# Optimization experiments

Hardware: AMD Instinct MI355X
Metric: run time of the kernel (lower is better)

## Reference

```python
import jax, jax.numpy as jnp
import numpy as np

B = 32768      # batch
D_RGB = 512    # resnet18 feature dim (fc.in_features)
D_SPD = 128    # speed branch width
D_IN = D_RGB + D_SPD  # 640
H = 256        # branch MLP hidden/out width
C = 7          # number of command branches


def setup_inputs() -> dict:
    key = jax.random.key(0)
    ks = jax.random.split(key, 24)
    s = 0.05
    n = jax.random.normal
    inp = {
        "rgb_feat": n(ks[0], (B, D_RGB), jnp.float32),
        "spd": n(ks[1], (B, 1), jnp.float32),
        "cmd": jax.random.randint(ks[2], (B,), 0, C, jnp.int32),
        # speed input MLP: 1 -> 128 -> 128 -> 128, tanh
        "spd_W1": n(ks[3], (1, D_SPD), jnp.float32) * s,
        "spd_b1": jnp.zeros((D_SPD,), jnp.float32),
        "spd_W2": n(ks[4], (D_SPD, D_SPD), jnp.float32) * s,
        "spd_b2": jnp.zeros((D_SPD,), jnp.float32),
        "spd_W3": n(ks[5], (D_SPD, D_SPD), jnp.float32) * s,
        "spd_b3": jnp.zeros((D_SPD,), jnp.float32),
        # 7 branch MLPs (stacked): 640 -> 256 -> 256 -> 256, sigmoid after each
        "W1": n(ks[6], (C, D_IN, H), jnp.float32) * s,
        "b1": jnp.zeros((C, H), jnp.float32),
        "W2": n(ks[7], (C, H, H), jnp.float32) * s,
        "b2": jnp.zeros((C, H), jnp.float32),
        "W3": n(ks[8], (C, H, H), jnp.float32) * s,
        "b3": jnp.zeros((C, H), jnp.float32),
        # per-branch heads: Linear(256,1) + sigmoid/tanh/sigmoid
        "hW_brk": n(ks[9], (C, H, 1), jnp.float32) * s,
        "hb_brk": jnp.zeros((C, 1), jnp.float32),
        "hW_str": n(ks[10], (C, H, 1), jnp.float32) * s,
        "hb_str": jnp.zeros((C, 1), jnp.float32),
        "hW_thr": n(ks[11], (C, H, 1), jnp.float32) * s,
        "hb_thr": jnp.zeros((C, 1), jnp.float32),
    }
    return inp


def reference(rgb_feat, spd, cmd,
              spd_W1, spd_b1, spd_W2, spd_b2, spd_W3, spd_b3,
              W1, b1, W2, b2, W3, b3,
              hW_brk, hb_brk, hW_str, hb_str, hW_thr, hb_thr):
    # speed input MLP (dropout = identity in eval)
    sfeat = jnp.tanh(spd @ spd_W1 + spd_b1)
    sfeat = jnp.tanh(sfeat @ spd_W2 + spd_b2)
    sfeat = jnp.tanh(sfeat @ spd_W3 + spd_b3)
    x = jnp.concatenate([rgb_feat, sfeat], axis=1)  # [B, 640]

    # Original computes every present branch's MLP on the FULL batch, then
    # gathers rows by command and scatter-sorts back. That is exactly
    # equivalent to: all-branch compute + per-row selection by cmd.
    h = jax.nn.sigmoid(jnp.einsum('bd,cdh->bch', x, W1) + b1)   # [B,C,H]
    h = jax.nn.sigmoid(jnp.einsum('bch,chk->bck', h, W2) + b2)
    h = jax.nn.sigmoid(jnp.einsum('bch,chk->bck', h, W3) + b3)
    sel = jnp.take_along_axis(h, cmd[:, None, None], axis=1)[:, 0]  # [B,H]

    def head(hW, hb, act):
        w = hW[cmd][:, :, 0]          # [B,H] per-row head weight
        b = hb[cmd][:, 0]             # [B]
        return act(jnp.sum(sel * w, axis=1) + b)[:, None]  # [B,1]

    brake = head(hW_brk, hb_brk, jax.nn.sigmoid)
    steer = head(hW_str, hb_str, jnp.tanh)
    throttle = head(hW_thr, hb_thr, jax.nn.sigmoid)
    return brake, steer, throttle
```

## Files before the change

### kernel.cpp

```cpp
#include <hip/hip_runtime.h>

#define B_N   32768
#define D_RGBc 512
#define D_SPDc 128
#define D_INc  640
#define Hc     256
#define Cc     7

typedef __bf16 bf16x8 __attribute__((ext_vector_type(8)));
typedef float  f32x4  __attribute__((ext_vector_type(4)));
typedef float  f32x16 __attribute__((ext_vector_type(16)));
typedef unsigned int u32;

__device__ __forceinline__ float sigmoidf_(float x) { return 1.0f / (1.0f + __expf(-x)); }
__device__ __forceinline__ float tanhf_(float x)    { float e = __expf(2.f * x); return (e - 1.f) / (e + 1.f); }

__device__ __forceinline__ u32 xoff(int row, int col) {
    return (u32)(((col >> 7) << 13) + (row << 8) + ((((col & 127) << 1)) ^ ((row & 15) << 4)));
}
__device__ __forceinline__ u32 soff(int row, int col) {
    return (u32)((row << 8) + (((col << 1)) ^ ((row & 15) << 4)));
}

__global__ void pack_kernel(const float* __restrict__ W1, const float* __restrict__ W2,
                            const float* __restrict__ W3, const float* __restrict__ sW2,
                            const float* __restrict__ sW3,
                            __bf16* __restrict__ p1, __bf16* __restrict__ p2,
                            __bf16* __restrict__ p3, __bf16* __restrict__ ps2,
                            __bf16* __restrict__ ps3, int* __restrict__ cnt)
{
    if (blockIdx.x == 0 && threadIdx.x < 16) cnt[threadIdx.x] = 0;
    int bid = blockIdx.x;
    const float* src; __bf16* dst; int K, N, nt, kc;
    if (bid < 560)      { int c = bid / 80, r = bid % 80; nt = r / 10; kc = r % 10;
        src = W1 + (size_t)c * D_INc * Hc; dst = p1 + (size_t)c * Hc * D_INc; K = D_INc; N = Hc; }
    else if (bid < 784) { int b = bid - 560; int c = b / 32, r = b % 32; nt = r / 4; kc = r % 4;
        src = W2 + (size_t)c * Hc * Hc; dst = p2 + (size_t)c * Hc * Hc; K = Hc; N = Hc; }
    else if (bid < 1008){ int b = bid - 784; int c = b / 32, r = b % 32; nt = r / 4; kc = r % 4;
        src = W3 + (size_t)c * Hc * Hc; dst = p3 + (size_t)c * Hc * Hc; K = Hc; N = Hc; }
    else if (bid < 1016){ int r = bid - 1008; nt = r / 2; kc = r % 2; src = sW2; dst = ps2; K = D_SPDc; N = D_SPDc; }
    else                { int r = bid - 1016; nt = r / 2; kc = r % 2; src = sW3; dst = ps3; K = D_SPDc; N = D_SPDc; }
    int k0 = kc * 64, n0 = nt * 32;
    __shared__ float tile[64][33];
    int t = threadIdx.x;
    int col = t & 31, r8 = (t >> 5) * 8;
    #pragma unroll
    for (int i = 0; i < 8; ++i)
        tile[r8 + i][col] = src[(size_t)(k0 + r8 + i) * N + n0 + col];
    __syncthreads();
    int ksl = t >> 6, lane = t & 63, l31 = lane & 31, hi = lane >> 5;
    bf16x8 v;
    #pragma unroll
    for (int j = 0; j < 8; ++j) v[j] = (__bf16)tile[ksl * 16 + hi * 8 + j][l31];
    *(bf16x8*)(dst + ((size_t)(nt * (K / 16) + (k0 >> 4) + ksl) * 64 + lane) * 8) = v;
}

__global__ void scatter_kernel(const int* __restrict__ cmd, int* __restrict__ cnt,
                               int* __restrict__ rowlist)
{
    int i = blockIdx.x * 256 + threadIdx.x;
    int lane = threadIdx.x & 63;
    int cv = cmd[i];
    #pragma unroll
    for (int c = 0; c < Cc; ++c) {
        unsigned long long m = __ballot(cv == c);
        if (!m) continue;
        int leader = __ffsll(m) - 1;
        int basep = 0;
        if (lane == leader) basep = atomicAdd(&cnt[c], (int)__popcll(m));
        basep = __shfl(basep, leader);
        if (cv == c) {
            int rank = (int)__popcll(m & ((1ull << lane) - 1ull));
            rowlist[c * B_N + basep + rank] = i;
        }
    }
}

__launch_bounds__(256, 3)
__global__ void branch_mlp_kernel(
    const float* __restrict__ rgb, const float* __restrict__ spd,
    const float* __restrict__ sW1, const float* __restrict__ sb1,
    const float* __restrict__ sb2, const float* __restrict__ sb3,
    const __bf16* __restrict__ ps2, const __bf16* __restrict__ ps3,
    const __bf16* __restrict__ p1, const __bf16* __restrict__ p2, const __bf16* __restrict__ p3,
    const float* __restrict__ b1, const float* __restrict__ b2, const float* __restrict__ b3,
    const float* __restrict__ hWb, const float* __restrict__ hbb,
    const float* __restrict__ hWs, const float* __restrict__ hbs,
    const float* __restrict__ hWt, const float* __restrict__ hbt,
    const int* __restrict__ cnt, const int* __restrict__ rowlist,
    float* __restrict__ out)
{
    __shared__ char xt[5 * 8192];
    __shared__ char sbuf[8192];
    __shared__ float headbuf[4][32][3];

    int bid = blockIdx.x;
    int c = -1, g = 0, accg = 0;
    #pragma unroll
    for (int i = 0; i < Cc; ++i) {
        int gc = (cnt[i] + 31) >> 5;
        if (c < 0 && bid < accg + gc) { c = i; g = bid - accg; }
        accg += gc;
    }
    if (c < 0) return;
    int n_c = cnt[c];
    const int* rl = rowlist + c * B_N;

    int tid = threadIdx.x, wave = tid >> 6, lane = tid & 63, l31 = lane & 31, hi = lane >> 5;

    int col0 = wave * 64 + l31, col1 = col0 + 32;
    float bv1a = b1[c * Hc + col0], bv1b = b1[c * Hc + col1];
    float bv2a = b2[c * Hc + col0], bv2b = b2[c * Hc + col1];
    float bv3a = b3[c * Hc + col0], bv3b = b3[c * Hc + col1];
    float wbA = hWb[c * Hc + col0], wbB = hWb[c * Hc + col1];
    float wsA = hWs[c * Hc + col0], wsB = hWs[c * Hc + col1];
    float wtA = hWt[c * Hc + col0], wtB = hWt[c * Hc + col1];
    float sb2v = sb2[wave * 32 + l31], sb3v = sb3[wave * 32 + l31];

    int r_st = tid >> 3, sub = tid & 7;
    int gg = g * 32 + r_st;
    int rid_st = rl[gg < n_c ? gg : n_c - 1];
    float sv = spd[rid_st];

    {
        int j0 = sub * 16;
        #pragma unroll
        for (int jj = 0; jj < 16; ++jj) {
            int j = j0 + jj;
            *(__bf16*)(sbuf + soff(r_st, j)) = (__bf16)tanhf_(sv * sW1[j] + sb1[j]);
        }
    }
    __syncthreads();

    f32x16 sacc;

    #pragma unroll
    for (int j = 0; j < 16; ++j) sacc[j] = 0.f;
    {
        const __bf16* pw = ps2 + ((size_t)(wave * 8) * 64 + lane) * 8;
        #pragma unroll
        for (int ks = 0; ks < 8; ++ks) {
            bf16x8 a = *(const bf16x8*)(sbuf + soff(l31, ks * 16 + hi * 8));
            bf16x8 b = *(const bf16x8*)(pw + (size_t)ks * 512);
            sacc = __builtin_amdgcn_mfma_f32_32x32x16_bf16(a, b, sacc, 0, 0, 0);
        }
    }
    __syncthreads();
    {
        int col = wave * 32 + l31;
        #pragma unroll
        for (int rg = 0; rg < 16; ++rg) {
            int row = (rg & 3) + 8 * (rg >> 2) + 4 * hi;
            *(__bf16*)(sbuf + soff(row, col)) = (__bf16)tanhf_(sacc[rg] + sb2v);
        }
    }
    __syncthreads();

    #pragma unroll
    for (int j = 0; j < 16; ++j) sacc[j] = 0.f;
    {
        const __bf16* pw = ps3 + ((size_t)(wave * 8) * 64 + lane) * 8;
        #pragma unroll
        for (int ks = 0; ks < 8; ++ks) {
            bf16x8 a = *(const bf16x8*)(sbuf + soff(l31, ks * 16 + hi * 8));
            bf16x8 b = *(const bf16x8*)(pw + (size_t)ks * 512);
            sacc = __builtin_amdgcn_mfma_f32_32x32x16_bf16(a, b, sacc, 0, 0, 0);
        }
    }
    {
        int col = wave * 32 + l31;
        #pragma unroll
        for (int rg = 0; rg < 16; ++rg) {
            int row = (rg & 3) + 8 * (rg >> 2) + 4 * hi;
            *(__bf16*)(xt + xoff(row, 512 + col)) = (__bf16)tanhf_(sacc[rg] + sb3v);
        }
    }

    {
        const float* rr = rgb + (size_t)rid_st * D_RGBc + sub * 8;
        #pragma unroll
        for (int i = 0; i < 8; ++i) {
            f32x4 v0 = *(const f32x4*)(rr + i * 64);
            f32x4 v1 = *(const f32x4*)(rr + i * 64 + 4);
            bf16x8 o;
            #pragma unroll
            for (int j = 0; j < 4; ++j) { o[j] = (__bf16)v0[j]; o[4 + j] = (__bf16)v1[j]; }
            *(bf16x8*)(xt + xoff(r_st, i * 64 + sub * 8)) = o;
        }
    }
    __syncthreads();

    f32x16 acc0, acc1;
    #pragma unroll
    for (int j = 0; j < 16; ++j) { acc0[j] = 0.f; acc1[j] = 0.f; }

    {
        const __bf16* pb = p1 + (size_t)c * Hc * D_INc;
        const __bf16* pw0 = pb + ((size_t)((2 * wave) * 40) * 64 + lane) * 8;
        const __bf16* pw1 = pb + ((size_t)((2 * wave + 1) * 40) * 64 + lane) * 8;
        #pragma unroll 8
        for (int ks = 0; ks < 40; ++ks) {
            bf16x8 a  = *(const bf16x8*)(xt + xoff(l31, ks * 16 + hi * 8));
            bf16x8 b0 = *(const bf16x8*)(pw0 + (size_t)ks * 512);
            bf16x8 b1v = *(const bf16x8*)(pw1 + (size_t)ks * 512);
            acc0 = __builtin_amdgcn_mfma_f32_32x32x16_bf16(a, b0, acc0, 0, 0, 0);
            acc1 = __builtin_amdgcn_mfma_f32_32x32x16_bf16(a, b1v, acc1, 0, 0, 0);
        }
    }
    __syncthreads();
    #pragma unroll
    for (int nt = 0; nt < 2; ++nt) {
        int col = wave * 64 + nt * 32 + l31;
        float bv = nt ? bv1b : bv1a;
        const f32x16& a = nt ? acc1 : acc0;
        #pragma unroll
        for (int rg = 0; rg < 16; ++rg) {
            int row = (rg & 3) + 8 * (rg >> 2) + 4 * hi;
            *(__bf16*)(xt + xoff(row, col)) = (__bf16)sigmoidf_(a[rg] + bv);
        }
    }
    __syncthreads();

    #pragma unroll
    for (int j = 0; j < 16; ++j) { acc0[j] = 0.f; acc1[j] = 0.f; }
    {
        const __bf16* pb = p2 + (size_t)c * Hc * Hc;
        const __bf16* pw0 = pb + ((size_t)((2 * wave) * 16) * 64 + lane) * 8;
        const __bf16* pw1 = pb + ((size_t)((2 * wave + 1) * 16) * 64 + lane) * 8;
        #pragma unroll
        for (int ks = 0; ks < 16; ++ks) {
            bf16x8 a  = *(const bf16x8*)(xt + xoff(l31, ks * 16 + hi * 8));
            bf16x8 b0 = *(const bf16x8*)(pw0 + (size_t)ks * 512);
            bf16x8 b1v = *(const bf16x8*)(pw1 + (size_t)ks * 512);
            acc0 = __builtin_amdgcn_mfma_f32_32x32x16_bf16(a, b0, acc0, 0, 0, 0);
            acc1 = __builtin_amdgcn_mfma_f32_32x32x16_bf16(a, b1v, acc1, 0, 0, 0);
        }
    }
    __syncthreads();
    #pragma unroll
    for (int nt = 0; nt < 2; ++nt) {
        int col = wave * 64 + nt * 32 + l31;
        float bv = nt ? bv2b : bv2a;
        const f32x16& a = nt ? acc1 : acc0;
        #pragma unroll
        for (int rg = 0; rg < 16; ++rg) {
            int row = (rg & 3) + 8 * (rg >> 2) + 4 * hi;
            *(__bf16*)(xt + xoff(row, col)) = (__bf16)sigmoidf_(a[rg] + bv);
        }
    }
    __syncthreads();

    #pragma unroll
    for (int j = 0; j < 16; ++j) { acc0[j] = 0.f; acc1[j] = 0.f; }
    {
        const __bf16* pb = p3 + (size_t)c * Hc * Hc;
        const __bf16* pw0 = pb + ((size_t)((2 * wave) * 16) * 64 + lane) * 8;
        const __bf16* pw1 = pb + ((size_t)((2 * wave + 1) * 16) * 64 + lane) * 8;
        #pragma unroll
        for (int ks = 0; ks < 16; ++ks) {
            bf16x8 a  = *(const bf16x8*)(xt + xoff(l31, ks * 16 + hi * 8));
            bf16x8 b0 = *(const bf16x8*)(pw0 + (size_t)ks * 512);
            bf16x8 b1v = *(const bf16x8*)(pw1 + (size_t)ks * 512);
            acc0 = __builtin_amdgcn_mfma_f32_32x32x16_bf16(a, b0, acc0, 0, 0, 0);
            acc1 = __builtin_amdgcn_mfma_f32_32x32x16_bf16(a, b1v, acc1, 0, 0, 0);
        }
    }

    float pr[3][16];
    #pragma unroll
    for (int hd = 0; hd < 3; ++hd)
        #pragma unroll
        for (int rg = 0; rg < 16; ++rg) pr[hd][rg] = 0.f;
    #pragma unroll
    for (int nt = 0; nt < 2; ++nt) {
        float bv = nt ? bv3b : bv3a;
        float wb = nt ? wbB : wbA, wsv = nt ? wsB : wsA, wtv = nt ? wtB : wtA;
        const f32x16& a = nt ? acc1 : acc0;
        #pragma unroll
        for (int rg = 0; rg < 16; ++rg) {
            float h = sigmoidf_(a[rg] + bv);
            pr[0][rg] += h * wb;
            pr[1][rg] += h * wsv;
            pr[2][rg] += h * wtv;
        }
    }
    #pragma unroll
    for (int m = 1; m < 32; m <<= 1)
        #pragma unroll
        for (int hd = 0; hd < 3; ++hd)
            #pragma unroll
            for (int rg = 0; rg < 16; ++rg)
                pr[hd][rg] += __shfl_xor(pr[hd][rg], m);
    if (l31 == 0) {
        #pragma unroll
        for (int rg = 0; rg < 16; ++rg) {
            int row = (rg & 3) + 8 * (rg >> 2) + 4 * hi;
            headbuf[wave][row][0] = pr[0][rg];
            headbuf[wave][row][1] = pr[1][rg];
            headbuf[wave][row][2] = pr[2][rg];
        }
    }
    __syncthreads();
    if (tid < 96) {
        int row = tid / 3, hd = tid % 3;
        int g2 = g * 32 + row;
        if (g2 < n_c) {
            int R = rl[g2];
            float v = headbuf[0][row][hd] + headbuf[1][row][hd] + headbuf[2][row][hd] + headbuf[3][row][hd];
            if (hd == 0)      out[R]           = sigmoidf_(v + hbb[c]);
            else if (hd == 1) out[B_N + R]     = tanhf_(v + hbs[c]);
            else              out[2 * B_N + R] = sigmoidf_(v + hbt[c]);
        }
    }
}

extern "C" void kernel_launch(void* const* d_in, const int* in_sizes, int n_in,
                              void* d_out, int out_size, void* d_ws, size_t ws_size,
                              hipStream_t stream)
{
    const float* rgb = (const float*)d_in[0];
    const float* spd = (const float*)d_in[1];
    const int*   cmd = (const int*)d_in[2];
    const float* sW1 = (const float*)d_in[3];
    const float* sb1 = (const float*)d_in[4];
    const float* sW2 = (const float*)d_in[5];
    const float* sb2 = (const float*)d_in[6];
    const float* sW3 = (const float*)d_in[7];
    const float* sb3 = (const float*)d_in[8];
    const float* W1  = (const float*)d_in[9];
    const float* b1  = (const float*)d_in[10];
    const float* W2  = (const float*)d_in[11];
    const float* b2  = (const float*)d_in[12];
    const float* W3  = (const float*)d_in[13];
    const float* b3  = (const float*)d_in[14];
    const float* hWb = (const float*)d_in[15];
    const float* hbb = (const float*)d_in[16];
    const float* hWs = (const float*)d_in[17];
    const float* hbs = (const float*)d_in[18];
    const float* hWt = (const float*)d_in[19];
    const float* hbt = (const float*)d_in[20];

    char* ws = (char*)d_ws;
    size_t off = 0;
    auto take = [&](size_t bytes) { char* p = ws + off; off = (off + bytes + 255) & ~(size_t)255; return p; };
    __bf16* p1  = (__bf16*)take((size_t)Cc * Hc * D_INc * 2);
    __bf16* p2  = (__bf16*)take((size_t)Cc * Hc * Hc * 2);
    __bf16* p3  = (__bf16*)take((size_t)Cc * Hc * Hc * 2);
    __bf16* ps2 = (__bf16*)take((size_t)D_SPDc * D_SPDc * 2);
    __bf16* ps3 = (__bf16*)take((size_t)D_SPDc * D_SPDc * 2);
    int* rowlist = (int*)take((size_t)Cc * B_N * 4);
    int* cnt     = (int*)take(16 * 4);

    pack_kernel<<<1024, 256, 0, stream>>>(W1, W2, W3, sW2, sW3, p1, p2, p3, ps2, ps3, cnt);
    scatter_kernel<<<128, 256, 0, stream>>>(cmd, cnt, rowlist);
    branch_mlp_kernel<<<1031, 256, 0, stream>>>(rgb, spd, sW1, sb1, sb2, sb3,
        ps2, ps3, p1, p2, p3, b1, b2, b3,
        hWb, hbb, hWs, hbs, hWt, hbt, cnt, rowlist, (float*)d_out);
}
```

Baseline: 231.8 us.

## Use 64-row tiles with 8 waves, pipelined rgb staging, and LDS head reduction

The branch MLP kernel now processes 64 gathered rows per workgroup with 512 threads instead of 32 rows with 256 threads. Each weight fragment loaded from global memory therefore feeds two MFMAs (one per 32-row half), halving weight traffic per row. The rgb input is loaded in 128-column chunks into registers and written to double-buffered LDS while the layer-1 MFMA loop runs on the previous chunk, overlapping the gather latency with compute. Block IDs are remapped across eight groups, and the final head dot products are computed from LDS with an 8-lane shuffle reduction instead of full-wave shuffles. The trade-offs are higher LDS usage (about 67 KB) and half as many workgroups, which may reduce occupancy and leave more padding waste on partial tiles.

```diff
diff --git a/kernel.cpp b/kernel.cpp
--- a/kernel.cpp
+++ b/kernel.cpp
@@ -14,13 +14,7 @@
 
 __device__ __forceinline__ float sigmoidf_(float x) { return 1.0f / (1.0f + __expf(-x)); }
 __device__ __forceinline__ float tanhf_(float x)    { float e = __expf(2.f * x); return (e - 1.f) / (e + 1.f); }
-
-__device__ __forceinline__ u32 xoff(int row, int col) {
-    return (u32)(((col >> 7) << 13) + (row << 8) + ((((col & 127) << 1)) ^ ((row & 15) << 4)));
-}
-__device__ __forceinline__ u32 soff(int row, int col) {
-    return (u32)((row << 8) + (((col << 1)) ^ ((row & 15) << 4)));
-}
+__device__ __forceinline__ u32 sw16(int row, int colbyte) { return (u32)(colbyte ^ ((row & 15) << 4)); }
 
 __global__ void pack_kernel(const float* __restrict__ W1, const float* __restrict__ W2,
                             const float* __restrict__ W3, const float* __restrict__ sW2,
@@ -76,7 +70,7 @@
     }
 }
 
-__launch_bounds__(256, 3)
+__launch_bounds__(512, 4)
 __global__ void branch_mlp_kernel(
     const float* __restrict__ rgb, const float* __restrict__ spd,
     const float* __restrict__ sW1, const float* __restrict__ sb1,
@@ -90,15 +84,17 @@
     const int* __restrict__ cnt, const int* __restrict__ rowlist,
     float* __restrict__ out)
 {
-    __shared__ char xt[5 * 8192];
-    __shared__ char sbuf[8192];
-    __shared__ float headbuf[4][32][3];
-
-    int bid = blockIdx.x;
+    __shared__ char lds[68608];
+    float* wld = (float*)(lds + 65536);
+
+    int nwg = gridDim.x;
+    int q = nwg >> 3;
+    int bid = (blockIdx.x & 7) * q + (blockIdx.x >> 3);
+
     int c = -1, g = 0, accg = 0;
     #pragma unroll
     for (int i = 0; i < Cc; ++i) {
-        int gc = (cnt[i] + 31) >> 5;
+        int gc = (cnt[i] + 63) >> 6;
         if (c < 0 && bid < accg + gc) { c = i; g = bid - accg; }
         accg += gc;
     }
@@ -108,208 +104,263 @@
 
     int tid = threadIdx.x, wave = tid >> 6, lane = tid & 63, l31 = lane & 31, hi = lane >> 5;
 
-    int col0 = wave * 64 + l31, col1 = col0 + 32;
-    float bv1a = b1[c * Hc + col0], bv1b = b1[c * Hc + col1];
-    float bv2a = b2[c * Hc + col0], bv2b = b2[c * Hc + col1];
-    float bv3a = b3[c * Hc + col0], bv3b = b3[c * Hc + col1];
-    float wbA = hWb[c * Hc + col0], wbB = hWb[c * Hc + col1];
-    float wsA = hWs[c * Hc + col0], wsB = hWs[c * Hc + col1];
-    float wtA = hWt[c * Hc + col0], wtB = hWt[c * Hc + col1];
-    float sb2v = sb2[wave * 32 + l31], sb3v = sb3[wave * 32 + l31];
+    for (int i = tid; i < 768; i += 512) {
+        const float* hw = (i < 256) ? hWb : (i < 512) ? hWs : hWt;
+        wld[i] = hw[c * Hc + (i & 255)];
+    }
 
     int r_st = tid >> 3, sub = tid & 7;
-    int gg = g * 32 + r_st;
-    int rid_st = rl[gg < n_c ? gg : n_c - 1];
+    int rowidx = g * 64 + r_st;
+    int rid_st = rl[rowidx < n_c ? rowidx : n_c - 1];
+    const float* rr = rgb + (size_t)rid_st * D_RGBc;
     float sv = spd[rid_st];
+
+    f32x4 La0 = *(const f32x4*)(rr + sub * 16);
+    f32x4 La1 = *(const f32x4*)(rr + sub * 16 + 4);
+    f32x4 La2 = *(const f32x4*)(rr + sub * 16 + 8);
+    f32x4 La3 = *(const f32x4*)(rr + sub * 16 + 12);
+    f32x4 Lb0 = *(const f32x4*)(rr + 128 + sub * 16);
+    f32x4 Lb1 = *(const f32x4*)(rr + 128 + sub * 16 + 4);
+    f32x4 Lb2 = *(const f32x4*)(rr + 128 + sub * 16 + 8);
+    f32x4 Lb3 = *(const f32x4*)(rr + 128 + sub * 16 + 12);
 
     {
         int j0 = sub * 16;
         #pragma unroll
         for (int jj = 0; jj < 16; ++jj) {
             int j = j0 + jj;
-            *(__bf16*)(sbuf + soff(r_st, j)) = (__bf16)tanhf_(sv * sW1[j] + sb1[j]);
-        }
-    }
-    __syncthreads();
+            *(__bf16*)(lds + 32768 + (r_st << 8) + sw16(r_st, (j << 1))) = (__bf16)tanhf_(sv * sW1[j] + sb1[j]);
+        }
+    }
+    {
+        bf16x8 o;
+        #pragma unroll
+        for (int j = 0; j < 4; ++j) { o[j] = (__bf16)La0[j]; o[4 + j] = (__bf16)La1[j]; }
+        *(bf16x8*)(lds + (r_st << 8) + sw16(r_st, (sub * 16) << 1)) = o;
+        #pragma unroll
+        for (int j = 0; j < 4; ++j) { o[j] = (__bf16)La2[j]; o[4 + j] = (__bf16)La3[j]; }
+        *(bf16x8*)(lds + (r_st << 8) + sw16(r_st, (sub * 16 + 8) << 1)) = o;
+    }
+    __syncthreads();
+
+    int mt = wave >> 2, nt = wave & 3;
+    int srowA = mt * 32 + l31;
 
     f32x16 sacc;
-
     #pragma unroll
     for (int j = 0; j < 16; ++j) sacc[j] = 0.f;
     {
-        const __bf16* pw = ps2 + ((size_t)(wave * 8) * 64 + lane) * 8;
+        const __bf16* pw = ps2 + ((size_t)(nt * 8) * 64 + lane) * 8;
         #pragma unroll
         for (int ks = 0; ks < 8; ++ks) {
-            bf16x8 a = *(const bf16x8*)(sbuf + soff(l31, ks * 16 + hi * 8));
+            bf16x8 a = *(const bf16x8*)(lds + 32768 + (srowA << 8) + sw16(srowA, (ks * 16 + hi * 8) << 1));
             bf16x8 b = *(const bf16x8*)(pw + (size_t)ks * 512);
             sacc = __builtin_amdgcn_mfma_f32_32x32x16_bf16(a, b, sacc, 0, 0, 0);
         }
     }
-    __syncthreads();
-    {
-        int col = wave * 32 + l31;
+    {
+        int col = nt * 32 + l31;
+        float bv = sb2[col];
         #pragma unroll
         for (int rg = 0; rg < 16; ++rg) {
-            int row = (rg & 3) + 8 * (rg >> 2) + 4 * hi;
-            *(__bf16*)(sbuf + soff(row, col)) = (__bf16)tanhf_(sacc[rg] + sb2v);
-        }
-    }
+            int row = mt * 32 + (rg & 3) + 8 * (rg >> 2) + 4 * hi;
+            *(__bf16*)(lds + 49152 + (row << 8) + sw16(row, col << 1)) = (__bf16)tanhf_(sacc[rg] + bv);
+        }
+    }
+    La0 = *(const f32x4*)(rr + 256 + sub * 16);
+    La1 = *(const f32x4*)(rr + 256 + sub * 16 + 4);
+    La2 = *(const f32x4*)(rr + 256 + sub * 16 + 8);
+    La3 = *(const f32x4*)(rr + 256 + sub * 16 + 12);
     __syncthreads();
 
     #pragma unroll
     for (int j = 0; j < 16; ++j) sacc[j] = 0.f;
     {
-        const __bf16* pw = ps3 + ((size_t)(wave * 8) * 64 + lane) * 8;
+        const __bf16* pw = ps3 + ((size_t)(nt * 8) * 64 + lane) * 8;
         #pragma unroll
         for (int ks = 0; ks < 8; ++ks) {
-            bf16x8 a = *(const bf16x8*)(sbuf + soff(l31, ks * 16 + hi * 8));
+            bf16x8 a = *(const bf16x8*)(lds + 49152 + (srowA << 8) + sw16(srowA, (ks * 16 + hi * 8) << 1));
             bf16x8 b = *(const bf16x8*)(pw + (size_t)ks * 512);
             sacc = __builtin_amdgcn_mfma_f32_32x32x16_bf16(a, b, sacc, 0, 0, 0);
         }
     }
     {
-        int col = wave * 32 + l31;
+        int col = nt * 32 + l31;
+        float bv = sb3[col];
         #pragma unroll
         for (int rg = 0; rg < 16; ++rg) {
-            int row = (rg & 3) + 8 * (rg >> 2) + 4 * hi;
-            *(__bf16*)(xt + xoff(row, 512 + col)) = (__bf16)tanhf_(sacc[rg] + sb3v);
-        }
-    }
-
-    {
-        const float* rr = rgb + (size_t)rid_st * D_RGBc + sub * 8;
-        #pragma unroll
-        for (int i = 0; i < 8; ++i) {
-            f32x4 v0 = *(const f32x4*)(rr + i * 64);
-            f32x4 v1 = *(const f32x4*)(rr + i * 64 + 4);
-            bf16x8 o;
+            int row = mt * 32 + (rg & 3) + 8 * (rg >> 2) + 4 * hi;
+            *(__bf16*)(lds + 32768 + (row << 8) + sw16(row, col << 1)) = (__bf16)tanhf_(sacc[rg] + bv);
+        }
+    }
+    {
+        bf16x8 o;
+        #pragma unroll
+        for (int j = 0; j < 4; ++j) { o[j] = (__bf16)Lb0[j]; o[4 + j] = (__bf16)Lb1[j]; }
+        *(bf16x8*)(lds + 16384 + (r_st << 8) + sw16(r_st, (sub * 16) << 1)) = o;
+        #pragma unroll
+        for (int j = 0; j < 4; ++j) { o[j] = (__bf16)Lb2[j]; o[4 + j] = (__bf16)Lb3[j]; }
+        *(bf16x8*)(lds + 16384 + (r_st << 8) + sw16(r_st, (sub * 16 + 8) << 1)) = o;
+    }
+    Lb0 = *(const f32x4*)(rr + 384 + sub * 16);
+    Lb1 = *(const f32x4*)(rr + 384 + sub * 16 + 4);
+    Lb2 = *(const f32x4*)(rr + 384 + sub * 16 + 8);
+    Lb3 = *(const f32x4*)(rr + 384 + sub * 16 + 12);
+    __syncthreads();
+
+    f32x16 acc0, acc1;
+    #pragma unroll
+    for (int j = 0; j < 16; ++j) { acc0[j] = 0.f; acc1[j] = 0.f; }
+    int rowA0 = l31, rowA1 = 32 + l31;
+    const __bf16* p1w = p1 + (size_t)c * Hc * D_INc + ((size_t)(wave * 40) * 64 + lane) * 8;
+
+    #define L1_CHUNK(BUFB, KF0)                                                              \
+    {                                                                                        \
+        _Pragma("unroll")                                                                    \
+        for (int ks = 0; ks < 8; ++ks) {                                                     \
+            bf16x8 a0 = *(const bf16x8*)(lds + (BUFB) + (rowA0 << 8) + sw16(rowA0, (ks * 16 + hi * 8) << 1)); \
+            bf16x8 a1 = *(const bf16x8*)(lds + (BUFB) + (rowA1 << 8) + sw16(rowA1, (ks * 16 + hi * 8) << 1)); \
+            bf16x8 b = *(const bf16x8*)(p1w + (size_t)((KF0) + ks) * 512);                   \
+            acc0 = __builtin_amdgcn_mfma_f32_32x32x16_bf16(a0, b, acc0, 0, 0, 0);            \
+            acc1 = __builtin_amdgcn_mfma_f32_32x32x16_bf16(a1, b, acc1, 0, 0, 0);            \
+        }                                                                                    \
+    }
+
+    L1_CHUNK(0, 0)
+    __syncthreads();
+    L1_CHUNK(16384, 8)
+    {
+        bf16x8 o;
+        #pragma unroll
+        for (int j = 0; j < 4; ++j) { o[j] = (__bf16)La0[j]; o[4 + j] = (__bf16)La1[j]; }
+        *(bf16x8*)(lds + (r_st << 8) + sw16(r_st, (sub * 16) << 1)) = o;
+        #pragma unroll
+        for (int j = 0; j < 4; ++j) { o[j] = (__bf16)La2[j]; o[4 + j] = (__bf16)La3[j]; }
+        *(bf16x8*)(lds + (r_st << 8) + sw16(r_st, (sub * 16 + 8) << 1)) = o;
+    }
+    __syncthreads();
+    L1_CHUNK(0, 16)
+    {
+        bf16x8 o;
+        #pragma unroll
+        for (int j = 0; j < 4; ++j) { o[j] = (__bf16)Lb0[j]; o[4 + j] = (__bf16)Lb1[j]; }
+        *(bf16x8*)(lds + 16384 + (r_st << 8) + sw16(r_st, (sub * 16) << 1)) = o;
+        #pragma unroll
+        for (int j = 0; j < 4; ++j) { o[j] = (__bf16)Lb2[j]; o[4 + j] = (__bf16)Lb3[j]; }
+        *(bf16x8*)(lds + 16384 + (r_st << 8) + sw16(r_st, (sub * 16 + 8) << 1)) = o;
+    }
+    __syncthreads();
+    L1_CHUNK(16384, 24)
+    {
+        #pragma unroll
+        for (int ks = 0; ks < 8; ++ks) {
+            bf16x8 a0 = *(const bf16x8*)(lds + 32768 + (rowA0 << 8) + sw16(rowA0, (ks * 16 + hi * 8) << 1));
+            bf16x8 a1 = *(const bf16x8*)(lds + 32768 + (rowA1 << 8) + sw16(rowA1, (ks * 16 + hi * 8) << 1));
+            bf16x8 b = *(const bf16x8*)(p1w + (size_t)(32 + ks) * 512);
+            acc0 = __builtin_amdgcn_mfma_f32_32x32x16_bf16(a0, b, acc0, 0, 0, 0);
+            acc1 = __builtin_amdgcn_mfma_f32_32x32x16_bf16(a1, b, acc1, 0, 0, 0);
+        }
+    }
+    __syncthreads();
+
+    int colW = wave * 32 + l31;
+    {
+        float bv = b1[c * Hc + colW];
+        int cb = (colW >> 7) << 14, cl = (colW & 127) << 1;
+        #pragma unroll
+        for (int rg = 0; rg < 16; ++rg) {
+            int row0 = (rg & 3) + 8 * (rg >> 2) + 4 * hi;
+            *(__bf16*)(lds + cb + (row0 << 8) + sw16(row0, cl)) = (__bf16)sigmoidf_(acc0[rg] + bv);
+            int row1 = 32 + row0;
+            *(__bf16*)(lds + cb + (row1 << 8) + sw16(row1, cl)) = (__bf16)sigmoidf_(acc1[rg] + bv);
+        }
+    }
+    __syncthreads();
+
+    #pragma unroll
+    for (int j = 0; j < 16; ++j) { acc0[j] = 0.f; acc1[j] = 0.f; }
+    {
+        const __bf16* p2w = p2 + (size_t)c * Hc * Hc + ((size_t)(wave * 16) * 64 + lane) * 8;
+        #pragma unroll
+        for (int ks = 0; ks < 16; ++ks) {
+            int kcol = ks * 16 + hi * 8;
+            int cb = (kcol >> 7) << 14, cl = (kcol & 127) << 1;
+            bf16x8 a0 = *(const bf16x8*)(lds + cb + (rowA0 << 8) + sw16(rowA0, cl));
+            bf16x8 a1 = *(const bf16x8*)(lds + cb + (rowA1 << 8) + sw16(rowA1, cl));
+            bf16x8 b = *(const bf16x8*)(p2w + (size_t)ks * 512);
+            acc0 = __builtin_amdgcn_mfma_f32_32x32x16_bf16(a0, b, acc0, 0, 0, 0);
+            acc1 = __builtin_amdgcn_mfma_f32_32x32x16_bf16(a1, b, acc1, 0, 0, 0);
+        }
+    }
+    {
+        float bv = b2[c * Hc + colW];
+        int cb = 32768 + ((colW >> 7) << 14), cl = (colW & 127) << 1;
+        #pragma unroll
+        for (int rg = 0; rg < 16; ++rg) {
+            int row0 = (rg & 3) + 8 * (rg >> 2) + 4 * hi;
+            *(__bf16*)(lds + cb + (row0 << 8) + sw16(row0, cl)) = (__bf16)sigmoidf_(acc0[rg] + bv);
+            int row1 = 32 + row0;
+            *(__bf16*)(lds + cb + (row1 << 8) + sw16(row1, cl)) = (__bf16)sigmoidf_(acc1[rg] + bv);
+        }
+    }
+    __syncthreads();
+
+    #pragma unroll
+    for (int j = 0; j < 16; ++j) { acc0[j] = 0.f; acc1[j] = 0.f; }
+    {
+        const __bf16* p3w = p3 + (size_t)c * Hc * Hc + ((size_t)(wave * 16) * 64 + lane) * 8;
+        #pragma unroll
+        for (int ks = 0; ks < 16; ++ks) {
+            int kcol = ks * 16 + hi * 8;
+            int cb = 32768 + ((kcol >> 7) << 14), cl = (kcol & 127) << 1;
+            bf16x8 a0 = *(const bf16x8*)(lds + cb + (rowA0 << 8) + sw16(rowA0, cl));
+            bf16x8 a1 = *(const bf16x8*)(lds + cb + (rowA1 << 8) + sw16(rowA1, cl));
+            bf16x8 b = *(const bf16x8*)(p3w + (size_t)ks * 512);
+            acc0 = __builtin_amdgcn_mfma_f32_32x32x16_bf16(a0, b, acc0, 0, 0, 0);
+            acc1 = __builtin_amdgcn_mfma_f32_32x32x16_bf16(a1, b, acc1, 0, 0, 0);
+        }
+    }
+    {
+        float bv = b3[c * Hc + colW];
+        int cb = (colW >> 7) << 14, cl = (colW & 127) << 1;
+        #pragma unroll
+        for (int rg = 0; rg < 16; ++rg) {
+            int row0 = (rg & 3) + 8 * (rg >> 2) + 4 * hi;
+            *(__bf16*)(lds + cb + (row0 << 8) + sw16(row0, cl)) = (__bf16)sigmoidf_(acc0[rg] + bv);
+            int row1 = 32 + row0;
+            *(__bf16*)(lds + cb + (row1 << 8) + sw16(row1, cl)) = (__bf16)sigmoidf_(acc1[rg] + bv);
+        }
+    }
+    __syncthreads();
+
+    {
+        int row = r_st, t8 = sub;
+        float pr0 = 0.f, pr1 = 0.f, pr2 = 0.f;
+        #pragma unroll
+        for (int q2 = 0; q2 < 4; ++q2) {
+            int col0 = t8 * 32 + q2 * 8;
+            int cb = (col0 >> 7) << 14, cl = (col0 & 127) << 1;
+            bf16x8 hv = *(const bf16x8*)(lds + cb + (row << 8) + sw16(row, cl));
             #pragma unroll
-            for (int j = 0; j < 4; ++j) { o[j] = (__bf16)v0[j]; o[4 + j] = (__bf16)v1[j]; }
-            *(bf16x8*)(xt + xoff(r_st, i * 64 + sub * 8)) = o;
-        }
-    }
-    __syncthreads();
-
-    f32x16 acc0, acc1;
-    #pragma unroll
-    for (int j = 0; j < 16; ++j) { acc0[j] = 0.f; acc1[j] = 0.f; }
-
-    {
-        const __bf16* pb = p1 + (size_t)c * Hc * D_INc;
-        const __bf16* pw0 = pb + ((size_t)((2 * wave) * 40) * 64 + lane) * 8;
-        const __bf16* pw1 = pb + ((size_t)((2 * wave + 1) * 40) * 64 + lane) * 8;
-        #pragma unroll 8
-        for (int ks = 0; ks < 40; ++ks) {
-            bf16x8 a  = *(const bf16x8*)(xt + xoff(l31, ks * 16 + hi * 8));
-            bf16x8 b0 = *(const bf16x8*)(pw0 + (size_t)ks * 512);
-            bf16x8 b1v = *(const bf16x8*)(pw1 + (size_t)ks * 512);
-            acc0 = __builtin_amdgcn_mfma_f32_32x32x16_bf16(a, b0, acc0, 0, 0, 0);
-            acc1 = __builtin_amdgcn_mfma_f32_32x32x16_bf16(a, b1v, acc1, 0, 0, 0);
-        }
-    }
-    __syncthreads();
-    #pragma unroll
-    for (int nt = 0; nt < 2; ++nt) {
-        int col = wave * 64 + nt * 32 + l31;
-        float bv = nt ? bv1b : bv1a;
-        const f32x16& a = nt ? acc1 : acc0;
-        #pragma unroll
-        for (int rg = 0; rg < 16; ++rg) {
-            int row = (rg & 3) + 8 * (rg >> 2) + 4 * hi;
-            *(__bf16*)(xt + xoff(row, col)) = (__bf16)sigmoidf_(a[rg] + bv);
-        }
-    }
-    __syncthreads();
-
-    #pragma unroll
-    for (int j = 0; j < 16; ++j) { acc0[j] = 0.f; acc1[j] = 0.f; }
-    {
-        const __bf16* pb = p2 + (size_t)c * Hc * Hc;
-        const __bf16* pw0 = pb + ((size_t)((2 * wave) * 16) * 64 + lane) * 8;
-        const __bf16* pw1 = pb + ((size_t)((2 * wave + 1) * 16) * 64 + lane) * 8;
-        #pragma unroll
-        for (int ks = 0; ks < 16; ++ks) {
-            bf16x8 a  = *(const bf16x8*)(xt + xoff(l31, ks * 16 + hi * 8));
-            bf16x8 b0 = *(const bf16x8*)(pw0 + (size_t)ks * 512);
-            bf16x8 b1v = *(const bf16x8*)(pw1 + (size_t)ks * 512);
-            acc0 = __builtin_amdgcn_mfma_f32_32x32x16_bf16(a, b0, acc0, 0, 0, 0);
-            acc1 = __builtin_amdgcn_mfma_f32_32x32x16_bf16(a, b1v, acc1, 0, 0, 0);
-        }
-    }
-    __syncthreads();
-    #pragma unroll
-    for (int nt = 0; nt < 2; ++nt) {
-        int col = wave * 64 + nt * 32 + l31;
-        float bv = nt ? bv2b : bv2a;
-        const f32x16& a = nt ? acc1 : acc0;
-        #pragma unroll
-        for (int rg = 0; rg < 16; ++rg) {
-            int row = (rg & 3) + 8 * (rg >> 2) + 4 * hi;
-            *(__bf16*)(xt + xoff(row, col)) = (__bf16)sigmoidf_(a[rg] + bv);
-        }
-    }
-    __syncthreads();
-
-    #pragma unroll
-    for (int j = 0; j < 16; ++j) { acc0[j] = 0.f; acc1[j] = 0.f; }
-    {
-        const __bf16* pb = p3 + (size_t)c * Hc * Hc;
-        const __bf16* pw0 = pb + ((size_t)((2 * wave) * 16) * 64 + lane) * 8;
-        const __bf16* pw1 = pb + ((size_t)((2 * wave + 1) * 16) * 64 + lane) * 8;
-        #pragma unroll
-        for (int ks = 0; ks < 16; ++ks) {
-            bf16x8 a  = *(const bf16x8*)(xt + xoff(l31, ks * 16 + hi * 8));
-            bf16x8 b0 = *(const bf16x8*)(pw0 + (size_t)ks * 512);
-            bf16x8 b1v = *(const bf16x8*)(pw1 + (size_t)ks * 512);
-            acc0 = __builtin_amdgcn_mfma_f32_32x32x16_bf16(a, b0, acc0, 0, 0, 0);
-            acc1 = __builtin_amdgcn_mfma_f32_32x32x16_bf16(a, b1v, acc1, 0, 0, 0);
-        }
-    }
-
-    float pr[3][16];
-    #pragma unroll
-    for (int hd = 0; hd < 3; ++hd)
-        #pragma unroll
-        for (int rg = 0; rg < 16; ++rg) pr[hd][rg] = 0.f;
-    #pragma unroll
-    for (int nt = 0; nt < 2; ++nt) {
-        float bv = nt ? bv3b : bv3a;
-        float wb = nt ? wbB : wbA, wsv = nt ? wsB : wsA, wtv = nt ? wtB : wtA;
-        const f32x16& a = nt ? acc1 : acc0;
-        #pragma unroll
-        for (int rg = 0; rg < 16; ++rg) {
-            float h = sigmoidf_(a[rg] + bv);
-            pr[0][rg] += h * wb;
-            pr[1][rg] += h * wsv;
-            pr[2][rg] += h * wtv;
-        }
-    }
-    #pragma unroll
-    for (int m = 1; m < 32; m <<= 1)
-        #pragma unroll
-        for (int hd = 0; hd < 3; ++hd)
-            #pragma unroll
-            for (int rg = 0; rg < 16; ++rg)
-                pr[hd][rg] += __shfl_xor(pr[hd][rg], m);
-    if (l31 == 0) {
-        #pragma unroll
-        for (int rg = 0; rg < 16; ++rg) {
-            int row = (rg & 3) + 8 * (rg >> 2) + 4 * hi;
-            headbuf[wave][row][0] = pr[0][rg];
-            headbuf[wave][row][1] = pr[1][rg];
-            headbuf[wave][row][2] = pr[2][rg];
-        }
-    }
-    __syncthreads();
-    if (tid < 96) {
-        int row = tid / 3, hd = tid % 3;
-        int g2 = g * 32 + row;
-        if (g2 < n_c) {
-            int R = rl[g2];
-            float v = headbuf[0][row][hd] + headbuf[1][row][hd] + headbuf[2][row][hd] + headbuf[3][row][hd];
-            if (hd == 0)      out[R]           = sigmoidf_(v + hbb[c]);
-            else if (hd == 1) out[B_N + R]     = tanhf_(v + hbs[c]);
-            else              out[2 * B_N + R] = sigmoidf_(v + hbt[c]);
+            for (int e = 0; e < 8; ++e) {
+                float h = (float)hv[e];
+                int col = col0 + e;
+                pr0 += h * wld[col];
+                pr1 += h * wld[256 + col];
+                pr2 += h * wld[512 + col];
+            }
+        }
+        #pragma unroll
+        for (int m = 1; m < 8; m <<= 1) {
+            pr0 += __shfl_xor(pr0, m);
+            pr1 += __shfl_xor(pr1, m);
+            pr2 += __shfl_xor(pr2, m);
+        }
+        if (t8 == 0 && rowidx < n_c) {
+            int R = rid_st;
+            out[R]           = sigmoidf_(pr0 + hbb[c]);
+            out[B_N + R]     = tanhf_(pr1 + hbs[c]);
+            out[2 * B_N + R] = sigmoidf_(pr2 + hbt[c]);
         }
     }
 }
@@ -353,7 +404,7 @@
 
     pack_kernel<<<1024, 256, 0, stream>>>(W1, W2, W3, sW2, sW3, p1, p2, p3, ps2, ps3, cnt);
     scatter_kernel<<<128, 256, 0, stream>>>(cmd, cnt, rowlist);
-    branch_mlp_kernel<<<1031, 256, 0, stream>>>(rgb, spd, sW1, sb1, sb2, sb3,
+    branch_mlp_kernel<<<520, 512, 0, stream>>>(rgb, spd, sW1, sb1, sb2, sb3,
         ps2, ps3, p1, p2, p3, b1, b2, b3,
         hWb, hbb, hWs, hbs, hWt, hbt, cnt, rowlist, (float*)d_out);
 }
```

After: 241.7 us. 4.3% more time.
